# Optimization experiments

Measured on AMD Instinct MI355X. Metric: run time of the kernel, lower is better.

## Reference

```python
import jax, jax.numpy as jnp
import numpy as np

DIM = 512
HEADS = 8


def setup_inputs() -> dict:
    key = jax.random.key(0)
    ks = jax.random.split(key, 9)
    s = 1.0 / np.sqrt(DIM)
    x = jax.random.normal(ks[0], (2, 4096, DIM), dtype=jnp.float32)
    Wq = jax.random.uniform(ks[1], (DIM, DIM), jnp.float32, -s, s)
    bq = jax.random.uniform(ks[2], (DIM,), jnp.float32, -s, s)
    Wk = jax.random.uniform(ks[3], (DIM, DIM), jnp.float32, -s, s)
    bk = jax.random.uniform(ks[4], (DIM,), jnp.float32, -s, s)
    Wv = jax.random.uniform(ks[5], (DIM, DIM), jnp.float32, -s, s)
    bv = jax.random.uniform(ks[6], (DIM,), jnp.float32, -s, s)
    Wo = jax.random.uniform(ks[7], (DIM, DIM), jnp.float32, -s, s)
    bo = jax.random.uniform(ks[8], (DIM,), jnp.float32, -s, s)
    return {"x": x, "Wq": Wq, "bq": bq, "Wk": Wk, "bk": bk,
            "Wv": Wv, "bv": bv, "Wo": Wo, "bo": bo}


def reference(x, Wq, bq, Wk, bk, Wv, bv, Wo, bo):
    b, t, d = x.shape
    h = HEADS
    dq = d // h
    scale = dq ** -0.5
    # projections: torch Linear is x @ W.T + b
    q = (x @ Wq.T + bq).reshape(b, t, h, dq)
    k = (x @ Wk.T + bk).reshape(b, t, h, dq)
    v = (x @ Wv.T + bv).reshape(b, t, h, dq)
    # attention scores [b, h, t, t] (full O(T^2) matrix, as in the original)
    att = jnp.einsum("bqhd,bkhd->bhqk", q, k) * scale
    att = jax.nn.softmax(att, axis=-1)
    out = jnp.einsum("bhqk,bkhd->bqhd", att, v).reshape(b, t, d)
    return out @ Wo.T + bo
```

## Files before the change

### kernel.cpp

```cpp
#include <hip/hip_runtime.h>

typedef short bf16x8 __attribute__((ext_vector_type(8)));
typedef float f32x4 __attribute__((ext_vector_type(4)));
typedef unsigned u32x2 __attribute__((ext_vector_type(2)));
typedef unsigned u32x4 __attribute__((ext_vector_type(4)));

#define MFMA(a, b, c) __builtin_amdgcn_mfma_f32_16x16x32_bf16((a), (b), (c), 0, 0, 0)

__device__ __forceinline__ unsigned cvtpk(float a, float b) {
    unsigned r;
    asm("v_cvt_pk_bf16_f32 %0, %1, %2" : "=v"(r) : "v"(a), "v"(b));
    return r;
}

__device__ __forceinline__ void gload16(const void* g, void* l) {
    __builtin_amdgcn_global_load_lds(
        (const __attribute__((address_space(1))) unsigned*)g,
        (__attribute__((address_space(3))) unsigned*)l, 16, 0, 0);
}

__global__ __launch_bounds__(256) void cvt_kernel(
    const float* __restrict__ x,
    const float* __restrict__ w0, const float* __restrict__ w1,
    const float* __restrict__ w2, const float* __restrict__ w3,
    unsigned short* __restrict__ xd,
    unsigned short* __restrict__ d0, unsigned short* __restrict__ d1,
    unsigned short* __restrict__ d2, unsigned short* __restrict__ d3)
{
    int bid = blockIdx.x;
    const float* src;
    unsigned short* dst;
    int off;
    if (bid < 4096) { src = x; dst = xd; off = bid; }
    else {
        int s = (bid - 4096) >> 8;
        src = s == 0 ? w0 : (s == 1 ? w1 : (s == 2 ? w2 : w3));
        dst = s == 0 ? d0 : (s == 1 ? d1 : (s == 2 ? d2 : d3));
        off = (bid - 4096) & 255;
    }
    size_t i = ((size_t)off * 256 + threadIdx.x) * 4;
    float4 v = *(const float4*)(src + i);
    uint2 pk;
    pk.x = cvtpk(v.x, v.y);
    pk.y = cvtpk(v.z, v.w);
    *(uint2*)(dst + i) = pk;
}

__device__ __forceinline__ void gemm128_core(
    const unsigned short* __restrict__ A, const unsigned short* __restrict__ W,
    int m0, int n0, int tid, unsigned short* sA, unsigned short* sB,
    f32x4 acc[4][4])
{
    const int lane = tid & 63, wid = tid >> 6;
    const int quad = lane >> 4, l15 = lane & 15;
    const int wm = wid >> 1, wn = wid & 1;

    const int gl_r = lane >> 3;
    const int gl_kc = (lane & 7) ^ gl_r;

    #pragma unroll
    for (int i = 0; i < 4; i++)
        #pragma unroll
        for (int j = 0; j < 4; j++) {
            f32x4 z = {0.f, 0.f, 0.f, 0.f};
            acc[i][j] = z;
        }

    for (int k0 = 0; k0 < 512; k0 += 64) {
        #pragma unroll
        for (int p = 0; p < 4; p++) {
            int chunk = wid * 4 + p;
            int row = chunk * 8 + gl_r;
            gload16(A + (size_t)(m0 + row) * 512 + k0 + gl_kc * 8,
                    (char*)sA + chunk * 1024);
            gload16(W + (size_t)(n0 + row) * 512 + k0 + gl_kc * 8,
                    (char*)sB + chunk * 1024);
        }
        __syncthreads();
        #pragma unroll
        for (int ks = 0; ks < 2; ks++) {
            bf16x8 af[4], bfr[4];
            #pragma unroll
            for (int i = 0; i < 4; i++) {
                int row = wm * 64 + i * 16 + l15;
                int kc = ks * 4 + quad;
                af[i] = *(const bf16x8*)((const char*)sA + row * 128 + ((kc ^ (row & 7)) << 4));
            }
            #pragma unroll
            for (int j = 0; j < 4; j++) {
                int row = wn * 64 + j * 16 + l15;
                int kc = ks * 4 + quad;
                bfr[j] = *(const bf16x8*)((const char*)sB + row * 128 + ((kc ^ (row & 7)) << 4));
            }
            #pragma unroll
            for (int i = 0; i < 4; i++)
                #pragma unroll
                for (int j = 0; j < 4; j++)
                    acc[i][j] = MFMA(af[i], bfr[j], acc[i][j]);
        }
        __syncthreads();
    }
}

__global__ __launch_bounds__(256) void qkv_kernel(
    const unsigned short* __restrict__ x,
    const unsigned short* __restrict__ Wq, const float* __restrict__ bq,
    const unsigned short* __restrict__ Wk, const float* __restrict__ bk,
    const unsigned short* __restrict__ Wv, const float* __restrict__ bv,
    unsigned short* __restrict__ qo, unsigned short* __restrict__ ko,
    unsigned short* __restrict__ vo)
{
    __shared__ unsigned short sA[128 * 64];
    __shared__ unsigned short sB[128 * 64];
    const int tid = threadIdx.x;
    const int by = blockIdx.y;
    const int sel = by >> 2;
    const int n0 = (by & 3) * 128;
    const int m0 = blockIdx.x * 128;
    const unsigned short* W = sel == 0 ? Wq : (sel == 1 ? Wk : Wv);
    const float* bias = sel == 0 ? bq : (sel == 1 ? bk : bv);

    f32x4 acc[4][4];
    gemm128_core(x, W, m0, n0, tid, sA, sB, acc);

    const int lane = tid & 63, wid = tid >> 6;
    const int quad = lane >> 4, l15 = lane & 15;
    const int wm = wid >> 1, wn = wid & 1;
    float bv4[4];
    #pragma unroll
    for (int j = 0; j < 4; j++) bv4[j] = bias[n0 + wn * 64 + j * 16 + l15];

    if (sel == 2) {
        #pragma unroll
        for (int i = 0; i < 4; i++) {
            #pragma unroll
            for (int j = 0; j < 4; j++) {
                int n = n0 + wn * 64 + j * 16 + l15;
                int h = n >> 6, d = n & 63;
                int m = m0 + wm * 64 + i * 16 + quad * 4;
                int b = m >> 12, t = m & 4095;
                uint2 pk;
                pk.x = cvtpk(acc[i][j][0] + bv4[j], acc[i][j][1] + bv4[j]);
                pk.y = cvtpk(acc[i][j][2] + bv4[j], acc[i][j][3] + bv4[j]);
                *(uint2*)(vo + ((size_t)(b * 8 + h) * 64 + d) * 4096 + t) = pk;
            }
        }
    } else {
        const float SC = (sel == 0) ? 0.125f * 1.44269504088896f : 1.0f;
        unsigned short* dst = sel == 0 ? qo : ko;
        #pragma unroll
        for (int i = 0; i < 4; i++) {
            #pragma unroll
            for (int j = 0; j < 4; j++) {
                int n = n0 + wn * 64 + j * 16 + l15;
                int h = n >> 6, d = n & 63;
                int m = m0 + wm * 64 + i * 16 + quad * 4;
                int b = m >> 12, t = m & 4095;
                size_t base2 = ((size_t)(b * 8 + h) * 4096 + t) * 64 + d;
                unsigned p01 = cvtpk((acc[i][j][0] + bv4[j]) * SC,
                                     (acc[i][j][1] + bv4[j]) * SC);
                unsigned p23 = cvtpk((acc[i][j][2] + bv4[j]) * SC,
                                     (acc[i][j][3] + bv4[j]) * SC);
                dst[base2]       = (unsigned short)p01;
                dst[base2 + 64]  = (unsigned short)(p01 >> 16);
                dst[base2 + 128] = (unsigned short)p23;
                dst[base2 + 192] = (unsigned short)(p23 >> 16);
            }
        }
    }
}

__global__ __launch_bounds__(512, 4) void attn_kernel(
    const unsigned short* __restrict__ qg, const unsigned short* __restrict__ kg,
    const unsigned short* __restrict__ vtg, unsigned short* __restrict__ og)
{
    __shared__ unsigned char smem[33280];

    const int tid = threadIdx.x;
    const int lane = tid & 63;
    const int w = tid >> 6;
    const int g = tid >> 8;
    const int gt = tid & 255;
    const int sw = w & 3;
    const int quad = lane >> 4, l15 = lane & 15;
    const int bh = blockIdx.y;
    const size_t base = (size_t)bh * 4096 * 64;
    const unsigned short* Q = qg + base;
    const unsigned short* K = kg + base;
    const unsigned short* VT = vtg + base;
    const int qt0 = blockIdx.x * 128;

    unsigned short* sK  = (unsigned short*)(smem + g * 8192);
    unsigned short* sVt = (unsigned short*)(smem + 16384 + g * 8192);

    bf16x8 qf[2][2];
    #pragma unroll
    for (int cb = 0; cb < 2; cb++) {
        int q = qt0 + sw * 32 + cb * 16 + l15;
        #pragma unroll
        for (int ks = 0; ks < 2; ks++)
            qf[cb][ks] = *(const bf16x8*)(Q + (size_t)q * 64 + ks * 32 + quad * 8);
    }

    f32x4 ot[4][2];
    #pragma unroll
    for (int i = 0; i < 4; i++)
        #pragma unroll
        for (int cb = 0; cb < 2; cb++) {
            f32x4 z = {0.f, 0.f, 0.f, 0.f};
            ot[i][cb] = z;
        }
    f32x4 ls[2];
    {
        f32x4 z = {0.f, 0.f, 0.f, 0.f};
        ls[0] = z; ls[1] = z;
    }
    const short one_b = (short)0x3F80;
    const bf16x8 ones = {one_b, one_b, one_b, one_b, one_b, one_b, one_b, one_b};

    const int c0 = gt, c1 = gt + 256;
    const int r0 = c0 >> 3, kc0 = c0 & 7;
    const int r1 = c1 >> 3, kc1 = c1 & 7;

    uint4 kr0, kr1, vr0, vr1;
    {
        int kb = g * 64;
        kr0 = *(const uint4*)(K + (size_t)(kb + r0) * 64 + kc0 * 8);
        kr1 = *(const uint4*)(K + (size_t)(kb + r1) * 64 + kc1 * 8);
        vr0 = *(const uint4*)(VT + (size_t)r0 * 4096 + kb + kc0 * 8);
        vr1 = *(const uint4*)(VT + (size_t)r1 * 4096 + kb + kc1 * 8);
    }

    for (int it = 0; it < 32; it++) {
        *(uint4*)((char*)sK + r0 * 128 + ((kc0 ^ (r0 & 7)) << 4)) = kr0;
        *(uint4*)((char*)sK + r1 * 128 + ((kc1 ^ (r1 & 7)) << 4)) = kr1;
        *(uint4*)((char*)sVt + r0 * 128 + ((kc0 ^ (r0 & 7)) << 4)) = vr0;
        *(uint4*)((char*)sVt + r1 * 128 + ((kc1 ^ (r1 & 7)) << 4)) = vr1;
        __syncthreads();

        {
            int itn = (it < 31) ? it + 1 : it;
            int kbn = (2 * itn + g) * 64;
            kr0 = *(const uint4*)(K + (size_t)(kbn + r0) * 64 + kc0 * 8);
            kr1 = *(const uint4*)(K + (size_t)(kbn + r1) * 64 + kc1 * 8);
            vr0 = *(const uint4*)(VT + (size_t)r0 * 4096 + kbn + kc0 * 8);
            vr1 = *(const uint4*)(VT + (size_t)r1 * 4096 + kbn + kc1 * 8);
        }

        #pragma unroll
        for (int half = 0; half < 2; half++) {
            unsigned xA[2], yA[2], zB[2], wB[2];
            #pragma unroll
            for (int rb2 = 0; rb2 < 2; rb2++) {
                int rb = half * 2 + rb2;
                int row = rb * 16 + l15;
                f32x4 s0 = {0.f, 0.f, 0.f, 0.f};
                f32x4 s1 = {0.f, 0.f, 0.f, 0.f};
                __builtin_amdgcn_s_setprio(1);
                #pragma unroll
                for (int ks = 0; ks < 2; ks++) {
                    int kc = ks * 4 + quad;
                    bf16x8 ka = *(const bf16x8*)((const char*)sK + row * 128 + ((kc ^ (row & 7)) << 4));
                    s0 = MFMA(ka, qf[0][ks], s0);
                    s1 = MFMA(ka, qf[1][ks], s1);
                }
                __builtin_amdgcn_s_setprio(0);
                unsigned e0 = cvtpk(__builtin_amdgcn_exp2f(s0[0]),
                                    __builtin_amdgcn_exp2f(s0[1]));
                unsigned e1 = cvtpk(__builtin_amdgcn_exp2f(s0[2]),
                                    __builtin_amdgcn_exp2f(s0[3]));
                unsigned f0 = cvtpk(__builtin_amdgcn_exp2f(s1[0]),
                                    __builtin_amdgcn_exp2f(s1[1]));
                unsigned f1 = cvtpk(__builtin_amdgcn_exp2f(s1[2]),
                                    __builtin_amdgcn_exp2f(s1[3]));
                if (rb2 == 0) { xA[0] = e0; yA[0] = e1; xA[1] = f0; yA[1] = f1; }
                else          { zB[0] = e0; wB[0] = e1; zB[1] = f0; wB[1] = f1; }
            }

            bf16x8 pf[2];
            #pragma unroll
            for (int cb = 0; cb < 2; cb++) {
                u32x2 s  = __builtin_amdgcn_permlane32_swap(xA[cb], zB[cb], false, false);
                u32x2 t  = __builtin_amdgcn_permlane16_swap(s[0], s[1], false, false);
                u32x2 s2 = __builtin_amdgcn_permlane32_swap(yA[cb], wB[cb], false, false);
                u32x2 t2 = __builtin_amdgcn_permlane16_swap(s2[0], s2[1], false, false);
                u32x4 fr = { t[0], t2[0], t[1], t2[1] };
                pf[cb] = __builtin_bit_cast(bf16x8, fr);
            }

            {
                int ks2 = half;
                __builtin_amdgcn_s_setprio(1);
                ls[0] = MFMA(ones, pf[0], ls[0]);
                ls[1] = MFMA(ones, pf[1], ls[1]);
                #pragma unroll
                for (int rbd = 0; rbd < 4; rbd++) {
                    int row = rbd * 16 + l15;
                    int kc = ks2 * 4 + quad;
                    bf16x8 vf = *(const bf16x8*)((const char*)sVt + row * 128 + ((kc ^ (row & 7)) << 4));
                    ot[rbd][0] = MFMA(vf, pf[0], ot[rbd][0]);
                    ot[rbd][1] = MFMA(vf, pf[1], ot[rbd][1]);
                }
                __builtin_amdgcn_s_setprio(0);
            }
        }
        __syncthreads();
    }

    float* oc = (float*)smem;
    float* lc = (float*)(smem + 32768);
    if (g == 1) {
        #pragma unroll
        for (int cb = 0; cb < 2; cb++) {
            int qb = sw * 32 + cb * 16 + l15;
            if (quad == 0) lc[qb] = ls[cb][0];
            #pragma unroll
            for (int rbd = 0; rbd < 4; rbd++) {
                int dc = rbd * 4 + quad;
                *(f32x4*)((char*)oc + qb * 256 + ((dc ^ (qb & 15)) << 4)) = ot[rbd][cb];
            }
        }
    }
    __syncthreads();
    if (g == 0) {
        const int b = bh >> 3, h = bh & 7;
        #pragma unroll
        for (int cb = 0; cb < 2; cb++) {
            int qb = sw * 32 + cb * 16 + l15;
            float inv = 1.f / (ls[cb][0] + lc[qb]);
            int q = qt0 + qb;
            #pragma unroll
            for (int rbd = 0; rbd < 4; rbd++) {
                int dc = rbd * 4 + quad;
                f32x4 o2 = *(const f32x4*)((char*)oc + qb * 256 + ((dc ^ (qb & 15)) << 4));
                uint2 pk;
                pk.x = cvtpk((ot[rbd][cb][0] + o2[0]) * inv,
                             (ot[rbd][cb][1] + o2[1]) * inv);
                pk.y = cvtpk((ot[rbd][cb][2] + o2[2]) * inv,
                             (ot[rbd][cb][3] + o2[3]) * inv);
                *(uint2*)(og + ((size_t)(b * 4096 + q) * 512 + h * 64 + rbd * 16 + quad * 4)) = pk;
            }
        }
    }
}

__global__ __launch_bounds__(256) void out_kernel(
    const unsigned short* __restrict__ attn,
    const unsigned short* __restrict__ Wo, const float* __restrict__ bo,
    float* __restrict__ out)
{
    __shared__ unsigned short sA[128 * 64];
    __shared__ unsigned short sB[128 * 64];
    const int tid = threadIdx.x;
    const int m0 = blockIdx.x * 128;
    const int n0 = blockIdx.y * 128;

    f32x4 acc[4][4];
    gemm128_core(attn, Wo, m0, n0, tid, sA, sB, acc);

    const int lane = tid & 63, wid = tid >> 6;
    const int quad = lane >> 4, l15 = lane & 15;
    const int wm = wid >> 1, wn = wid & 1;
    float bv4[4];
    #pragma unroll
    for (int j = 0; j < 4; j++) bv4[j] = bo[n0 + wn * 64 + j * 16 + l15];
    #pragma unroll
    for (int i = 0; i < 4; i++) {
        #pragma unroll
        for (int j = 0; j < 4; j++) {
            int n = n0 + wn * 64 + j * 16 + l15;
            #pragma unroll
            for (int r = 0; r < 4; r++) {
                int m = m0 + wm * 64 + i * 16 + quad * 4 + r;
                out[(size_t)m * 512 + n] = acc[i][j][r] + bv4[j];
            }
        }
    }
}

extern "C" void kernel_launch(void* const* d_in, const int* in_sizes, int n_in,
                              void* d_out, int out_size, void* d_ws, size_t ws_size,
                              hipStream_t stream) {
    const float* x  = (const float*)d_in[0];
    const float* Wq = (const float*)d_in[1];
    const float* bq = (const float*)d_in[2];
    const float* Wk = (const float*)d_in[3];
    const float* bk = (const float*)d_in[4];
    const float* Wv = (const float*)d_in[5];
    const float* bv = (const float*)d_in[6];
    const float* Wo = (const float*)d_in[7];
    const float* bo = (const float*)d_in[8];
    unsigned short* ws = (unsigned short*)d_ws;

    const size_t NTOK = (size_t)2 * 4096 * 512;
    const size_t WSZ = (size_t)512 * 512;
    unsigned short* xb  = ws;
    unsigned short* Wqb = ws + NTOK;
    unsigned short* Wkb = Wqb + WSZ;
    unsigned short* Wvb = Wkb + WSZ;
    unsigned short* Wob = Wvb + WSZ;
    unsigned short* q_ws = Wob + WSZ;
    unsigned short* k_ws = q_ws + NTOK;
    unsigned short* v_ws = k_ws + NTOK;
    unsigned short* a_ws = v_ws + NTOK;

    cvt_kernel<<<5120, 256, 0, stream>>>(x, Wq, Wk, Wv, Wo, xb, Wqb, Wkb, Wvb, Wob);
    qkv_kernel<<<dim3(64, 12), 256, 0, stream>>>(xb, Wqb, bq, Wkb, bk, Wvb, bv,
                                                 q_ws, k_ws, v_ws);
    attn_kernel<<<dim3(32, 16), 512, 0, stream>>>(q_ws, k_ws, v_ws, a_ws);
    out_kernel<<<dim3(64, 4), 256, 0, stream>>>(a_ws, Wob, bo,
                                                (float*)d_out);
}
```

Measured before the change: 194.5 us.

## Double-buffer K/V tiles in LDS via direct global-to-LDS async loads

Replaces the register-staged K and V^T prefetch with global_load_lds direct writes into a second LDS buffer. The next tile is fetched while the current one is computed, and the trailing barrier is dropped. The aim is to remove the VGPR staging and the LDS store instructions, and to overlap loads with MFMA work. LDS use doubles to about 66KB per block, which may lower occupancy below the 4 blocks requested by launch bounds.

```diff
diff --git a/kernel.cpp b/kernel.cpp
--- a/kernel.cpp
+++ b/kernel.cpp
@@ -174,13 +174,13 @@
     const unsigned short* __restrict__ qg, const unsigned short* __restrict__ kg,
     const unsigned short* __restrict__ vtg, unsigned short* __restrict__ og)
 {
-    __shared__ unsigned char smem[33280];
+    __shared__ unsigned char smem[66048];
 
     const int tid = threadIdx.x;
     const int lane = tid & 63;
     const int w = tid >> 6;
     const int g = tid >> 8;
-    const int gt = tid & 255;
+    const int wg = w & 3;
     const int sw = w & 3;
     const int quad = lane >> 4, l15 = lane & 15;
     const int bh = blockIdx.y;
@@ -190,8 +190,8 @@
     const unsigned short* VT = vtg + base;
     const int qt0 = blockIdx.x * 128;
 
-    unsigned short* sK  = (unsigned short*)(smem + g * 8192);
-    unsigned short* sVt = (unsigned short*)(smem + 16384 + g * 8192);
+    const int srow = lane >> 3;
+    const int skc  = (lane & 7) ^ srow;
 
     bf16x8 qf[2][2];
     #pragma unroll
@@ -218,34 +218,39 @@
     const short one_b = (short)0x3F80;
     const bf16x8 ones = {one_b, one_b, one_b, one_b, one_b, one_b, one_b, one_b};
 
-    const int c0 = gt, c1 = gt + 256;
-    const int r0 = c0 >> 3, kc0 = c0 & 7;
-    const int r1 = c1 >> 3, kc1 = c1 & 7;
-
-    uint4 kr0, kr1, vr0, vr1;
     {
         int kb = g * 64;
-        kr0 = *(const uint4*)(K + (size_t)(kb + r0) * 64 + kc0 * 8);
-        kr1 = *(const uint4*)(K + (size_t)(kb + r1) * 64 + kc1 * 8);
-        vr0 = *(const uint4*)(VT + (size_t)r0 * 4096 + kb + kc0 * 8);
-        vr1 = *(const uint4*)(VT + (size_t)r1 * 4096 + kb + kc1 * 8);
-    }
-
+        unsigned char* bK = smem + g * 8192;
+        unsigned char* bV = smem + 16384 + g * 8192;
+        #pragma unroll
+        for (int p = 0; p < 2; p++) {
+            int chunk = wg * 2 + p;
+            int row = chunk * 8 + srow;
+            gload16(K + (size_t)(kb + row) * 64 + skc * 8, bK + chunk * 1024);
+            gload16(VT + (size_t)row * 4096 + kb + skc * 8, bV + chunk * 1024);
+        }
+    }
+
+    int buf = 0;
     for (int it = 0; it < 32; it++) {
-        *(uint4*)((char*)sK + r0 * 128 + ((kc0 ^ (r0 & 7)) << 4)) = kr0;
-        *(uint4*)((char*)sK + r1 * 128 + ((kc1 ^ (r1 & 7)) << 4)) = kr1;
-        *(uint4*)((char*)sVt + r0 * 128 + ((kc0 ^ (r0 & 7)) << 4)) = vr0;
-        *(uint4*)((char*)sVt + r1 * 128 + ((kc1 ^ (r1 & 7)) << 4)) = vr1;
+        __asm__ __volatile__("s_waitcnt vmcnt(0)" ::: "memory");
         __syncthreads();
 
-        {
-            int itn = (it < 31) ? it + 1 : it;
-            int kbn = (2 * itn + g) * 64;
-            kr0 = *(const uint4*)(K + (size_t)(kbn + r0) * 64 + kc0 * 8);
-            kr1 = *(const uint4*)(K + (size_t)(kbn + r1) * 64 + kc1 * 8);
-            vr0 = *(const uint4*)(VT + (size_t)r0 * 4096 + kbn + kc0 * 8);
-            vr1 = *(const uint4*)(VT + (size_t)r1 * 4096 + kbn + kc1 * 8);
-        }
+        if (it < 31) {
+            int kb = (2 * (it + 1) + g) * 64;
+            unsigned char* bK = smem + (buf ^ 1) * 32768 + g * 8192;
+            unsigned char* bV = smem + (buf ^ 1) * 32768 + 16384 + g * 8192;
+            #pragma unroll
+            for (int p = 0; p < 2; p++) {
+                int chunk = wg * 2 + p;
+                int row = chunk * 8 + srow;
+                gload16(K + (size_t)(kb + row) * 64 + skc * 8, bK + chunk * 1024);
+                gload16(VT + (size_t)row * 4096 + kb + skc * 8, bV + chunk * 1024);
+            }
+        }
+
+        unsigned short* sK  = (unsigned short*)(smem + buf * 32768 + g * 8192);
+        unsigned short* sVt = (unsigned short*)(smem + buf * 32768 + 16384 + g * 8192);
 
         #pragma unroll
         for (int half = 0; half < 2; half++) {
@@ -304,11 +309,11 @@
                 __builtin_amdgcn_s_setprio(0);
             }
         }
-        __syncthreads();
+        buf ^= 1;
     }
 
     float* oc = (float*)smem;
-    float* lc = (float*)(smem + 32768);
+    float* lc = (float*)(smem + 65536);
     if (g == 1) {
         #pragma unroll
         for (int cb = 0; cb < 2; cb++) {
```

Result: faster. 189.7 us (-2.5%).
